# Optimization experiments

Measured on AMD Instinct MI355X. Metric: run time of the kernel, lower is better.

## Reference

```python
import jax, jax.numpy as jnp
from jax import lax
import numpy as np

H = 768          # BERT-base hidden size
NLAB = 2         # labelnum
T = NLAB + 2     # CRF tagset incl START/STOP (NCRF++ convention)
START = NLAB     # index 2
STOP = NLAB + 1  # index 3


def setup_inputs() -> dict:
    key = jax.random.key(0)
    ks = jax.random.split(key, 8)
    B, S1 = 64, 513  # S1 = 1 (CLS) + 512 content tokens
    emb = jax.random.normal(ks[0], (B, S1, H), dtype=jnp.float32)
    answer_seq_label = jax.random.randint(ks[1], (B, S1), 0, NLAB)
    IsQA = jax.random.randint(ks[2], (B,), 0, 2)
    fc2_W = jax.random.normal(ks[3], (2, H), dtype=jnp.float32) * 0.02
    fc2_b = jnp.zeros((2,), dtype=jnp.float32)
    crf_W = jax.random.normal(ks[4], (T, H), dtype=jnp.float32) * 0.02
    crf_b = jnp.zeros((T,), dtype=jnp.float32)
    transitions = jax.random.normal(ks[5], (T, T), dtype=jnp.float32) * 0.1
    return {"emb": emb, "answer_seq_label": answer_seq_label, "IsQA": IsQA,
            "fc2_W": fc2_W, "fc2_b": fc2_b, "crf_W": crf_W, "crf_b": crf_b,
            "transitions": transitions}


def _crf_log_partition(feats, trans):
    # feats [B,S,T]; linear-chain forward algorithm (log-sum-exp scan)
    alpha0 = feats[:, 0] + trans[START][None]           # [B,T]
    def step(alpha, feat_t):
        # alpha[b,prev] + trans[prev,cur] -> logsumexp over prev
        new = jax.nn.logsumexp(alpha[:, :, None] + trans[None], axis=1) + feat_t
        return new, None
    alpha, _ = lax.scan(step, alpha0, jnp.swapaxes(feats[:, 1:], 0, 1))
    return jax.nn.logsumexp(alpha + trans[:, STOP][None], axis=1)  # [B]


def _crf_gold_score(feats, tags, trans):
    # feats [B,S,T], tags [B,S]
    emit = jnp.take_along_axis(feats, tags[:, :, None], axis=2)[..., 0].sum(axis=1)
    tr = trans[tags[:, :-1], tags[:, 1:]].sum(axis=1)
    tr = tr + trans[START, tags[:, 0]] + trans[tags[:, -1], STOP]
    return emit + tr


def _crf_viterbi(feats, trans):
    # feats [B,S,T] -> best path [B,S]
    delta0 = feats[:, 0] + trans[START][None]
    def step(delta, feat_t):
        scores = delta[:, :, None] + trans[None]   # [B,prev,cur]
        bp = jnp.argmax(scores, axis=1)            # [B,T]
        return jnp.max(scores, axis=1) + feat_t, bp
    delta, bps = lax.scan(step, delta0, jnp.swapaxes(feats[:, 1:], 0, 1))  # bps [S-1,B,T]
    last_tag = jnp.argmax(delta + trans[:, STOP][None], axis=1)            # [B]
    def back(tag, bp_t):
        prev = jnp.take_along_axis(bp_t, tag[:, None], axis=1)[:, 0]
        return prev, prev
    _, path_prefix = lax.scan(back, last_tag, bps, reverse=True)           # [S-1,B]
    return jnp.concatenate([path_prefix, last_tag[None]], axis=0).T        # [B,S]


def reference(emb, answer_seq_label, IsQA, fc2_W, fc2_b, crf_W, crf_b, transitions):
    # CLS head + cross-entropy
    cls_emb = emb[:, 0]                              # [B,H]
    isqa_logits = cls_emb @ fc2_W.T + fc2_b          # [B,2]
    logp = jax.nn.log_softmax(isqa_logits, axis=-1)
    isqa_loss = -jnp.take_along_axis(logp, IsQA[:, None], axis=1).mean()
    isqa_pred = jnp.argmax(isqa_logits, axis=-1)[:, None]
    # CRF head (dropout = identity in eval); feats [B,S,T]
    feats = jnp.einsum('bsh,th->bst', emb[:, 1:], crf_W) + crf_b
    tags = answer_seq_label[:, 1:]
    Z = _crf_log_partition(feats, transitions)
    gold = _crf_gold_score(feats, tags, transitions)
    crf_loss = jnp.mean(Z - gold)
    crf_pred = _crf_viterbi(feats, transitions)
    return (isqa_pred, crf_pred, isqa_loss, crf_loss, tags, IsQA[:, None])
```

## Files before the change

kernel.cpp:

```cpp
#include <hip/hip_runtime.h>
#include <math.h>

#define B     64
#define S1    513
#define S     512
#define H     768
#define T     4
#define START 2
#define STOP  3

#define OUT_ISQA_PRED 0
#define OUT_CRF_PRED  64
#define OUT_ISQA_LOSS 32832
#define OUT_CRF_LOSS  32833
#define OUT_TAGS      32834
#define OUT_ISQA      65602

#define WS_FEATS  0
#define WS_LOGITS (B*S*T)
#define WS_ZG     (B*S*T + 2*B)

template<int CTRL>
__device__ __forceinline__ float dppf(float x) {
    int v = __builtin_amdgcn_update_dpp(__builtin_bit_cast(int, x),
                                        __builtin_bit_cast(int, x),
                                        CTRL, 0xF, 0xF, false);
    return __builtin_bit_cast(float, v);
}

__device__ __forceinline__ float lse4(float x0, float x1, float x2, float x3) {
    float m = fmaxf(fmaxf(x0, x1), fmaxf(x2, x3));
    return m + __logf(__expf(x0 - m) + __expf(x1 - m) +
                      __expf(x2 - m) + __expf(x3 - m));
}

__global__ __launch_bounds__(256) void feats_kernel(
    const float* __restrict__ emb,
    const float* __restrict__ fc2_W, const float* __restrict__ fc2_b,
    const float* __restrict__ crf_W, const float* __restrict__ crf_b,
    float* __restrict__ ws)
{
    __shared__ float wlds[6 * H];
    for (int i = threadIdx.x; i < 6 * H; i += 256)
        wlds[i] = (i < 4 * H) ? crf_W[i] : fc2_W[i - 4 * H];
    __syncthreads();

    const int tid  = threadIdx.x;
    const int lane = tid & 63;
    const int l8   = lane & 7;
    const int gw   = blockIdx.x * 4 + (tid >> 6);
    const int r    = gw * 8 + (lane >> 3);
    const int b    = r / S1;
    const int s    = r - b * S1;

    const float4* __restrict__ row4 = (const float4*)emb + (size_t)r * (H / 4);
    const float4* __restrict__ wl4  = (const float4*)wlds;
    const int o0 = s ? 0 * 192 : 4 * 192;
    const int o1 = s ? 1 * 192 : 5 * 192;
    const int o2 = s ? 2 * 192 : 4 * 192;
    const int o3 = s ? 3 * 192 : 5 * 192;

    float a0 = 0.f, a1 = 0.f, a2 = 0.f, a3 = 0.f;
    #pragma unroll 8
    for (int k = 0; k < 24; ++k) {
        const int idx = l8 + 8 * k;
        float4 e  = row4[idx];
        float4 w0 = wl4[o0 + idx];
        float4 w1 = wl4[o1 + idx];
        float4 w2 = wl4[o2 + idx];
        float4 w3 = wl4[o3 + idx];
        a0 += e.x * w0.x + e.y * w0.y + e.z * w0.z + e.w * w0.w;
        a1 += e.x * w1.x + e.y * w1.y + e.z * w1.z + e.w * w1.w;
        a2 += e.x * w2.x + e.y * w2.y + e.z * w2.z + e.w * w2.w;
        a3 += e.x * w3.x + e.y * w3.y + e.z * w3.z + e.w * w3.w;
    }
    a0 += dppf<0xB1>(a0); a0 += dppf<0x4E>(a0); a0 += __shfl_xor(a0, 4);
    a1 += dppf<0xB1>(a1); a1 += dppf<0x4E>(a1); a1 += __shfl_xor(a1, 4);
    a2 += dppf<0xB1>(a2); a2 += dppf<0x4E>(a2); a2 += __shfl_xor(a2, 4);
    a3 += dppf<0xB1>(a3); a3 += dppf<0x4E>(a3); a3 += __shfl_xor(a3, 4);

    if (l8 == 0) {
        if (s) {
            float4 o;
            o.x = a0 + crf_b[0]; o.y = a1 + crf_b[1];
            o.z = a2 + crf_b[2]; o.w = a3 + crf_b[3];
            ((float4*)(ws + WS_FEATS))[b * S + (s - 1)] = o;
        } else {
            ws[WS_LOGITS + 2 * b + 0] = a0 + fc2_b[0];
            ws[WS_LOGITS + 2 * b + 1] = a1 + fc2_b[1];
        }
    }
}

__global__ __launch_bounds__(256) void crf_kernel(
    const int* __restrict__ ans, const int* __restrict__ isqa,
    const float* __restrict__ trans,
    float* __restrict__ ws, float* __restrict__ out)
{
    __shared__ float smemf[10240];
    const int tid = threadIdx.x;
    const int blk = blockIdx.x;

    if (blk < 64) {
        const int b = blk;
        float* sf  = smemf;
        float* C   = smemf + 2048;
        float* red = smemf + 3072;

        float tr[16];
        #pragma unroll
        for (int i = 0; i < 16; ++i) tr[i] = trans[i];

        {
            float4* sf4 = (float4*)sf;
            const float4* src4 = (const float4*)(ws + WS_FEATS) + b * 512;
            sf4[tid] = src4[tid];
            sf4[tid + 256] = src4[tid + 256];
        }
        __syncthreads();

        float g = 0.f;
        #pragma unroll
        for (int u = 0; u < 2; ++u) {
            const int t   = 2 * tid + u;
            const int tag = ans[b * S1 + 1 + t];
            out[OUT_TAGS + b * S + t] = (float)tag;
            g += sf[t * 4 + tag];
            g += (t == 0) ? tr[START * 4 + tag] : tr[ans[b * S1 + t] * 4 + tag];
            if (t == S - 1) g += tr[tag * 4 + STOP];
        }
        #pragma unroll
        for (int m = 32; m; m >>= 1) g += __shfl_xor(g, m);
        if ((tid & 63) == 0) red[tid >> 6] = g;

        const int c  = tid >> 2;
        const int jr = tid & 3;
        const int t0 = c ? 8 * c : 1;
        float rl[4];
        #pragma unroll
        for (int i = 0; i < 4; ++i) rl[i] = tr[jr * 4 + i] + sf[t0 * 4 + i];
        for (int t = t0 + 1; t <= 8 * c + 7; ++t) {
            const float f0 = sf[t*4+0], f1 = sf[t*4+1], f2 = sf[t*4+2], f3 = sf[t*4+3];
            float nr[4];
            #pragma unroll
            for (int i = 0; i < 4; ++i)
                nr[i] = lse4(rl[0] + tr[0*4+i], rl[1] + tr[1*4+i],
                             rl[2] + tr[2*4+i], rl[3] + tr[3*4+i]);
            rl[0] = nr[0] + f0; rl[1] = nr[1] + f1;
            rl[2] = nr[2] + f2; rl[3] = nr[3] + f3;
        }
        ((float4*)C)[c * 4 + jr] = make_float4(rl[0], rl[1], rl[2], rl[3]);
        __syncthreads();

        for (int d = 1; d <= 32; d <<= 1) {
            const int cs = (c >= d) ? (c - d) : c;
            float4 ar = ((float4*)C)[cs * 4 + jr];
            float4 b0 = ((float4*)C)[c * 4 + 0];
            float4 b1 = ((float4*)C)[c * 4 + 1];
            float4 b2 = ((float4*)C)[c * 4 + 2];
            float4 b3 = ((float4*)C)[c * 4 + 3];
            __syncthreads();
            if (c >= d) {
                float4 nr;
                nr.x = lse4(ar.x + b0.x, ar.y + b1.x, ar.z + b2.x, ar.w + b3.x);
                nr.y = lse4(ar.x + b0.y, ar.y + b1.y, ar.z + b2.y, ar.w + b3.y);
                nr.z = lse4(ar.x + b0.z, ar.y + b1.z, ar.z + b2.z, ar.w + b3.z);
                nr.w = lse4(ar.x + b0.w, ar.y + b1.w, ar.z + b2.w, ar.w + b3.w);
                ((float4*)C)[c * 4 + jr] = nr;
            }
            __syncthreads();
        }

        if (tid == 0) {
            const float gold = red[0] + red[1] + red[2] + red[3];
            float a0k[4];
            #pragma unroll
            for (int k = 0; k < 4; ++k) a0k[k] = sf[k] + tr[START * 4 + k];
            const float* P = C + 63 * 16;
            float aN[4];
            #pragma unroll
            for (int i = 0; i < 4; ++i)
                aN[i] = lse4(a0k[0] + P[0*4+i], a0k[1] + P[1*4+i],
                             a0k[2] + P[2*4+i], a0k[3] + P[3*4+i]);
            const float Z = lse4(aN[0] + tr[0*4+STOP], aN[1] + tr[1*4+STOP],
                                 aN[2] + tr[2*4+STOP], aN[3] + tr[3*4+STOP]);
            ws[WS_ZG + b] = Z - gold;
            out[OUT_ISQA + b] = (float)isqa[b];
        }
    } else {
        const int bv = blk - 64;
        float* sfw = smemf;
        unsigned int* bpw = (unsigned int*)(smemf + 8192);
        {
            float4* d4 = (float4*)sfw;
            const float4* s4 = (const float4*)(ws + WS_FEATS) + bv * 4 * 512;
            #pragma unroll
            for (int n = 0; n < 8; ++n) d4[tid + 256 * n] = s4[tid + 256 * n];
        }
        if (tid < 4) bpw[tid * 512] = 0x03020100u;
        __syncthreads();

        const int w    = tid >> 6;
        const int lane = tid & 63;
        const int j    = lane & 3;
        const int b    = bv * 4 + w;
        const float* myf = sfw + w * 2048;
        unsigned char* mybp = (unsigned char*)(bpw + w * 512);

        const float tc0 = trans[0*4+j], tc1 = trans[1*4+j];
        const float tc2 = trans[2*4+j], tc3 = trans[3*4+j];
        const float tjs = trans[j*4 + STOP];

        float d = myf[j] + trans[START * 4 + j];
        float fcur = myf[4 + j];
        for (int t = 1; t < 512; ++t) {
            const float fnext = myf[(t + 1) * 4 + j];
            const float d0 = dppf<0x00>(d), d1 = dppf<0x55>(d);
            const float d2 = dppf<0xAA>(d), d3 = dppf<0xFF>(d);
            const float y0 = d0 + tc0, y1 = d1 + tc1;
            const float y2 = d2 + tc2, y3 = d3 + tc3;
            float bv01 = y0; int bi01 = 0;
            if (y1 > bv01) { bv01 = y1; bi01 = 1; }
            float bv23 = y2; int bi23 = 2;
            if (y3 > bv23) { bv23 = y3; bi23 = 3; }
            float bvv = bv01; int bi = bi01;
            if (bv23 > bvv) { bvv = bv23; bi = bi23; }
            d = bvv + fcur;
            fcur = fnext;
            if (lane < 4) mybp[t * 4 + j] = (unsigned char)bi;
        }

        const float vj = d + tjs;
        const float z0 = dppf<0x00>(vj), z1 = dppf<0x55>(vj);
        const float z2 = dppf<0xAA>(vj), z3 = dppf<0xFF>(vj);
        float m01 = z0; unsigned int i01 = 0;
        if (z1 > m01) { m01 = z1; i01 = 1; }
        float m23 = z2; unsigned int i23 = 2;
        if (z3 > m23) { m23 = z3; i23 = 3; }
        const unsigned int lt = (m23 > m01) ? i23 : i01;

        __syncthreads();

        const uint4 wv0 = ((const uint4*)(bpw + w * 512))[lane * 2 + 0];
        const uint4 wv1 = ((const uint4*)(bpw + w * 512))[lane * 2 + 1];
        unsigned int wk[8] = {wv0.x, wv0.y, wv0.z, wv0.w, wv1.x, wv1.y, wv1.z, wv1.w};
        unsigned int G = wk[7];
        #pragma unroll
        for (int k = 6; k >= 0; --k)
            G = __builtin_amdgcn_perm(0u, wk[k], G);
        unsigned int Sm = G;
        #pragma unroll
        for (int dd = 1; dd < 64; dd <<= 1) {
            const int srcl = lane + dd;
            const unsigned int oth = __shfl(Sm, (srcl < 64) ? srcl : 63);
            if (srcl < 64) Sm = __builtin_amdgcn_perm(0u, Sm, oth);
        }
        unsigned int emap = __shfl(Sm, (lane < 63) ? lane + 1 : 63);
        if (lane == 63) emap = 0x03020100u;
        unsigned int cur = (emap >> (8 * lt)) & 3u;

        float tg[8];
        tg[7] = (float)cur;
        #pragma unroll
        for (int k = 7; k >= 1; --k) {
            cur = (wk[k] >> (8 * cur)) & 3u;
            tg[k - 1] = (float)cur;
        }
        float4* op = (float4*)(out + OUT_CRF_PRED + b * S + lane * 8);
        op[0] = make_float4(tg[0], tg[1], tg[2], tg[3]);
        op[1] = make_float4(tg[4], tg[5], tg[6], tg[7]);
    }
}

__global__ __launch_bounds__(64) void final_kernel(
    const int* __restrict__ isqa, const float* __restrict__ ws,
    float* __restrict__ out)
{
    const int lane = threadIdx.x;
    const float zg = ws[WS_ZG + lane];
    const float l0 = ws[WS_LOGITS + lane * 2 + 0];
    const float l1 = ws[WS_LOGITS + lane * 2 + 1];
    const float m  = fmaxf(l0, l1);
    const float lse = m + __logf(__expf(l0 - m) + __expf(l1 - m));
    const int   y   = isqa[lane];
    const float li  = lse - (y ? l1 : l0);

    float s1 = zg, s2 = li;
    #pragma unroll
    for (int d = 32; d; d >>= 1) {
        s1 += __shfl_xor(s1, d);
        s2 += __shfl_xor(s2, d);
    }
    out[OUT_ISQA_PRED + lane] = (l1 > l0) ? 1.0f : 0.0f;
    if (lane == 0) {
        out[OUT_CRF_LOSS]  = s1 * (1.0f / 64.0f);
        out[OUT_ISQA_LOSS] = s2 * (1.0f / 64.0f);
    }
}

extern "C" void kernel_launch(void* const* d_in, const int* in_sizes, int n_in,
                              void* d_out, int out_size, void* d_ws, size_t ws_size,
                              hipStream_t stream)
{
    const float* emb    = (const float*)d_in[0];
    const int*   ans    = (const int*)d_in[1];
    const int*   isqa   = (const int*)d_in[2];
    const float* fc2_W  = (const float*)d_in[3];
    const float* fc2_b  = (const float*)d_in[4];
    const float* crf_W  = (const float*)d_in[5];
    const float* crf_b  = (const float*)d_in[6];
    const float* trans  = (const float*)d_in[7];
    float* out = (float*)d_out;
    float* ws  = (float*)d_ws;

    feats_kernel<<<1026, 256, 0, stream>>>(emb, fc2_W, fc2_b, crf_W, crf_b, ws);
    crf_kernel<<<80, 256, 0, stream>>>(ans, isqa, trans, ws, out);
    final_kernel<<<1, 64, 0, stream>>>(isqa, ws, out);
}
```

Measured before the change: 215.0 us.

## Fuse final reduction into CRF kernel via atomic counter; widen feats rows

Removes the separate final_kernel launch. The last of the 64 partition-function blocks, detected through an atomic counter in workspace that feats_kernel resets, now performs the loss reductions. The feats kernel assigns 16 lanes per row instead of 8, doubles the grid to 2052 blocks, and adds an occupancy hint to launch_bounds, aiming for more parallelism on the memory-bound projection. The cost is threadfence and atomic overhead plus a dependence on the counter reset ordering across launches.

```diff
diff --git a/kernel.cpp b/kernel.cpp
--- a/kernel.cpp
+++ b/kernel.cpp
@@ -19,6 +19,7 @@
 #define WS_FEATS  0
 #define WS_LOGITS (B*S*T)
 #define WS_ZG     (B*S*T + 2*B)
+#define WS_CNT    (B*S*T + 3*B)
 
 template<int CTRL>
 __device__ __forceinline__ float dppf(float x) {
@@ -34,7 +35,7 @@
                       __expf(x2 - m) + __expf(x3 - m));
 }
 
-__global__ __launch_bounds__(256) void feats_kernel(
+__global__ __launch_bounds__(256, 6) void feats_kernel(
     const float* __restrict__ emb,
     const float* __restrict__ fc2_W, const float* __restrict__ fc2_b,
     const float* __restrict__ crf_W, const float* __restrict__ crf_b,
@@ -43,13 +44,15 @@
     __shared__ float wlds[6 * H];
     for (int i = threadIdx.x; i < 6 * H; i += 256)
         wlds[i] = (i < 4 * H) ? crf_W[i] : fc2_W[i - 4 * H];
+    if (blockIdx.x == 0 && threadIdx.x == 0)
+        ((int*)ws)[WS_CNT] = 0;
     __syncthreads();
 
     const int tid  = threadIdx.x;
     const int lane = tid & 63;
-    const int l8   = lane & 7;
+    const int l16  = lane & 15;
     const int gw   = blockIdx.x * 4 + (tid >> 6);
-    const int r    = gw * 8 + (lane >> 3);
+    const int r    = gw * 4 + (lane >> 4);
     const int b    = r / S1;
     const int s    = r - b * S1;
 
@@ -61,9 +64,9 @@
     const int o3 = s ? 3 * 192 : 5 * 192;
 
     float a0 = 0.f, a1 = 0.f, a2 = 0.f, a3 = 0.f;
-    #pragma unroll 8
-    for (int k = 0; k < 24; ++k) {
-        const int idx = l8 + 8 * k;
+    #pragma unroll 4
+    for (int k = 0; k < 12; ++k) {
+        const int idx = l16 + 16 * k;
         float4 e  = row4[idx];
         float4 w0 = wl4[o0 + idx];
         float4 w1 = wl4[o1 + idx];
@@ -74,12 +77,16 @@
         a2 += e.x * w2.x + e.y * w2.y + e.z * w2.z + e.w * w2.w;
         a3 += e.x * w3.x + e.y * w3.y + e.z * w3.z + e.w * w3.w;
     }
-    a0 += dppf<0xB1>(a0); a0 += dppf<0x4E>(a0); a0 += __shfl_xor(a0, 4);
-    a1 += dppf<0xB1>(a1); a1 += dppf<0x4E>(a1); a1 += __shfl_xor(a1, 4);
-    a2 += dppf<0xB1>(a2); a2 += dppf<0x4E>(a2); a2 += __shfl_xor(a2, 4);
-    a3 += dppf<0xB1>(a3); a3 += dppf<0x4E>(a3); a3 += __shfl_xor(a3, 4);
-
-    if (l8 == 0) {
+    a0 += dppf<0xB1>(a0); a0 += dppf<0x4E>(a0);
+    a1 += dppf<0xB1>(a1); a1 += dppf<0x4E>(a1);
+    a2 += dppf<0xB1>(a2); a2 += dppf<0x4E>(a2);
+    a3 += dppf<0xB1>(a3); a3 += dppf<0x4E>(a3);
+    a0 += __shfl_xor(a0, 4); a0 += __shfl_xor(a0, 8);
+    a1 += __shfl_xor(a1, 4); a1 += __shfl_xor(a1, 8);
+    a2 += __shfl_xor(a2, 4); a2 += __shfl_xor(a2, 8);
+    a3 += __shfl_xor(a3, 4); a3 += __shfl_xor(a3, 8);
+
+    if (l16 == 0) {
         if (s) {
             float4 o;
             o.x = a0 + crf_b[0]; o.y = a1 + crf_b[1];
@@ -98,6 +105,7 @@
     float* __restrict__ ws, float* __restrict__ out)
 {
     __shared__ float smemf[10240];
+    __shared__ int isLast;
     const int tid = threadIdx.x;
     const int blk = blockIdx.x;
 
@@ -186,6 +194,32 @@
                                  aN[2] + tr[2*4+STOP], aN[3] + tr[3*4+STOP]);
             ws[WS_ZG + b] = Z - gold;
             out[OUT_ISQA + b] = (float)isqa[b];
+            __threadfence();
+            const int old = atomicAdd((int*)ws + WS_CNT, 1);
+            isLast = (old == 63);
+        }
+        __syncthreads();
+
+        if (isLast && tid < 64) {
+            __threadfence();
+            const float zg = ws[WS_ZG + tid];
+            const float l0 = ws[WS_LOGITS + tid * 2 + 0];
+            const float l1 = ws[WS_LOGITS + tid * 2 + 1];
+            const float m  = fmaxf(l0, l1);
+            const float lse = m + __logf(__expf(l0 - m) + __expf(l1 - m));
+            const int   y   = isqa[tid];
+            const float li  = lse - (y ? l1 : l0);
+            float s1 = zg, s2 = li;
+            #pragma unroll
+            for (int d = 32; d; d >>= 1) {
+                s1 += __shfl_xor(s1, d);
+                s2 += __shfl_xor(s2, d);
+            }
+            out[OUT_ISQA_PRED + tid] = (l1 > l0) ? 1.0f : 0.0f;
+            if (tid == 0) {
+                out[OUT_CRF_LOSS]  = s1 * (1.0f / 64.0f);
+                out[OUT_ISQA_LOSS] = s2 * (1.0f / 64.0f);
+            }
         }
     } else {
         const int bv = blk - 64;
@@ -272,32 +306,6 @@
     }
 }
 
-__global__ __launch_bounds__(64) void final_kernel(
-    const int* __restrict__ isqa, const float* __restrict__ ws,
-    float* __restrict__ out)
-{
-    const int lane = threadIdx.x;
-    const float zg = ws[WS_ZG + lane];
-    const float l0 = ws[WS_LOGITS + lane * 2 + 0];
-    const float l1 = ws[WS_LOGITS + lane * 2 + 1];
-    const float m  = fmaxf(l0, l1);
-    const float lse = m + __logf(__expf(l0 - m) + __expf(l1 - m));
-    const int   y   = isqa[lane];
-    const float li  = lse - (y ? l1 : l0);
-
-    float s1 = zg, s2 = li;
-    #pragma unroll
-    for (int d = 32; d; d >>= 1) {
-        s1 += __shfl_xor(s1, d);
-        s2 += __shfl_xor(s2, d);
-    }
-    out[OUT_ISQA_PRED + lane] = (l1 > l0) ? 1.0f : 0.0f;
-    if (lane == 0) {
-        out[OUT_CRF_LOSS]  = s1 * (1.0f / 64.0f);
-        out[OUT_ISQA_LOSS] = s2 * (1.0f / 64.0f);
-    }
-}
-
 extern "C" void kernel_launch(void* const* d_in, const int* in_sizes, int n_in,
                               void* d_out, int out_size, void* d_ws, size_t ws_size,
                               hipStream_t stream)
@@ -313,7 +321,6 @@
     float* out = (float*)d_out;
     float* ws  = (float*)d_ws;
 
-    feats_kernel<<<1026, 256, 0, stream>>>(emb, fc2_W, fc2_b, crf_W, crf_b, ws);
+    feats_kernel<<<2052, 256, 0, stream>>>(emb, fc2_W, fc2_b, crf_W, crf_b, ws);
     crf_kernel<<<80, 256, 0, stream>>>(ans, isqa, trans, ws, out);
-    final_kernel<<<1, 64, 0, stream>>>(isqa, ws, out);
-}
+}
```

After: 210.4 us. 2.2% less time.
